# Optimization experiments

Hardware: AMD Instinct MI355X
Metric: run time of the kernel (lower is better)

## Reference

```python
import jax, jax.numpy as jnp
import numpy as np

N_NODES = 10000
N_EDGES = 320000
F_IN = 128


def _mlp2(h, W1, b1, W2, b2):
    h = jax.nn.relu(h @ W1 + b1)
    return jax.nn.relu(h @ W2 + b2)


def edge_conv(x, src, dst, W1, b1, W2, b2, num_nodes):
    # DGCNN-style EdgeConv: per-edge message MLP(concat(x_i, x_j - x_i)), max-agg per node i
    xi = x[dst]                      # [E, F] center node features
    xj = x[src]                      # [E, F] neighbor features
    m = jnp.concatenate([xi, xj - xi], axis=-1)  # [E, 2F]
    h = _mlp2(m, W1, b1, W2, b2)     # [E, F_out]
    agg = jax.ops.segment_max(h, dst, num_segments=num_nodes)  # [N, F_out]
    # nodes with no incoming edges get -inf from segment_max; zero them
    return jnp.where(jnp.isfinite(agg), agg, 0.0)


def setup_inputs() -> dict:
    key = jax.random.key(0)
    ks = jax.random.split(key, 16)
    s = 0.05
    x = jax.random.normal(ks[0], (N_NODES, F_IN), dtype=jnp.float32)
    edge_index = jax.random.randint(ks[1], (2, N_EDGES), 0, N_NODES)
    # EdgeConvE 1: MLP(512, 256), input 2*128=256
    W1a = jax.random.normal(ks[2], (2 * F_IN, 512), dtype=jnp.float32) * s
    b1a = jnp.zeros((512,), dtype=jnp.float32)
    W2a = jax.random.normal(ks[3], (512, 256), dtype=jnp.float32) * s
    b2a = jnp.zeros((256,), dtype=jnp.float32)
    # EdgeConvE 2: MLP(256, 128), input 2*256=512
    W1b = jax.random.normal(ks[4], (512, 256), dtype=jnp.float32) * s
    b1b = jnp.zeros((256,), dtype=jnp.float32)
    W2b = jax.random.normal(ks[5], (256, 128), dtype=jnp.float32) * s
    b2b = jnp.zeros((128,), dtype=jnp.float32)
    # Dense head
    W3 = jax.random.normal(ks[6], (128, 64), dtype=jnp.float32) * s
    b3 = jnp.zeros((64,), dtype=jnp.float32)
    W4 = jax.random.normal(ks[7], (64, 1), dtype=jnp.float32) * s
    b4 = jnp.zeros((1,), dtype=jnp.float32)
    return {"x": x, "edge_index": edge_index,
            "W1a": W1a, "b1a": b1a, "W2a": W2a, "b2a": b2a,
            "W1b": W1b, "b1b": b1b, "W2b": W2b, "b2b": b2b,
            "W3": W3, "b3": b3, "W4": W4, "b4": b4}


def reference(x, edge_index, W1a, b1a, W2a, b2a, W1b, b1b, W2b, b2b, W3, b3, W4, b4):
    src, dst = edge_index[0], edge_index[1]
    h = edge_conv(x, src, dst, W1a, b1a, W2a, b2a, N_NODES)   # [N, 256]
    h = edge_conv(h, src, dst, W1b, b1b, W2b, b2b, N_NODES)   # [N, 128]
    h = jax.nn.relu(h @ W3 + b3)                               # [N, 64]
    return jax.nn.sigmoid(h @ W4 + b4)                         # [N, 1]
```

## Files before the change

kernel.cpp:

```cpp
#include <hip/hip_runtime.h>
#include <math.h>

#define NN 10000
#define NE 320000

typedef __attribute__((ext_vector_type(8))) short s8v;
typedef __attribute__((ext_vector_type(8))) _Float16 h8v;
typedef __attribute__((ext_vector_type(4))) float f4v;

__device__ __forceinline__ short f2h(float f) {
  _Float16 h = (_Float16)f;
  short s; __builtin_memcpy(&s, &h, 2); return s;
}
__device__ __forceinline__ uint4 cvt8(uint4 ua, uint4 ub) {
  h8v a, b;
  __builtin_memcpy(&a, &ua, 16);
  __builtin_memcpy(&b, &ub, 16);
  h8v r = a + b;
  r = __builtin_elementwise_max(r, (h8v)(_Float16)0.0f);
  uint4 o; __builtin_memcpy(&o, &r, 16);
  return o;
}

__global__ void hist_kernel(const int* __restrict__ ei, int* __restrict__ cnt) {
  int e = blockIdx.x * 256 + threadIdx.x;
  if (e < NE) atomicAdd(&cnt[ei[NE + e]], 1);
}

__global__ void __launch_bounds__(1024)
scan_kernel(const int* __restrict__ cnt, int* __restrict__ cur) {
  __shared__ int part[1024];
  const int t = threadIdx.x;
  const int base = t * 10;
  int local[10];
  int s = 0;
#pragma unroll
  for (int u = 0; u < 10; ++u) {
    int c = (base + u < NN) ? cnt[base + u] : 0;
    local[u] = s; s += c;
  }
  part[t] = s;
  __syncthreads();
  for (int off = 1; off < 1024; off <<= 1) {
    int v = part[t];
    int w = (t >= off) ? part[t - off] : 0;
    __syncthreads();
    part[t] = v + w;
    __syncthreads();
  }
  int excl = (t == 0) ? 0 : part[t - 1];
#pragma unroll
  for (int u = 0; u < 10; ++u)
    if (base + u < NN) cur[base + u] = excl + local[u];
}

__global__ void scatter_kernel(const int* __restrict__ ei, int* __restrict__ cur,
                               int* __restrict__ sSrc, int* __restrict__ sDst) {
  int e = blockIdx.x * 256 + threadIdx.x;
  if (e < NE) {
    int d = ei[NE + e];
    int p = atomicAdd(&cur[d], 1);
    sSrc[p] = ei[e];
    sDst[p] = d;
  }
}

__global__ void prep_weights(const float* __restrict__ W1a, const float* __restrict__ W1b,
                             const float* __restrict__ W2a, const float* __restrict__ W2b,
                             short* __restrict__ Wp1T, short* __restrict__ Wp2T,
                             short* __restrict__ BTf1, short* __restrict__ BTf2) {
  int i = blockIdx.x * 256 + threadIdx.x;
  if (i < 131072) {
    int j = i >> 7, k = i & 127;
    float v;
    if (j < 512) v = W1a[k * 512 + j] - W1a[(k + 128) * 512 + j];
    else         v = W1a[(k + 128) * 512 + (j - 512)];
    Wp1T[i] = f2h(v);
  } else if (i < 262144) {
    int t = i - 131072;
    int j = t >> 8, k = t & 255;
    float v;
    if (j < 256) v = W1b[k * 256 + j] - W1b[(k + 256) * 256 + j];
    else         v = W1b[(k + 256) * 256 + (j - 256)];
    Wp2T[t] = f2h(v);
  } else if (i < 393216) {
    int t = i - 262144;
    int n = t >> 9, k = t & 511;
    BTf1[(k >> 5) * 8192 + n * 32 + (k & 31)] = f2h(W2a[k * 256 + n]);
  } else if (i < 425984) {
    int t = i - 393216;
    int n = t >> 8, k = t & 255;
    BTf2[(k >> 5) * 4096 + n * 32 + (k & 31)] = f2h(W2b[k * 128 + n]);
  }
}

template<int K>
__global__ void __launch_bounds__(256)
node_gemm(const float* __restrict__ A, const short* __restrict__ BT,
          const float* __restrict__ bias, int biasLen,
          short* __restrict__ C, int Ntot) {
  const int rowBase = blockIdx.x * 64;
  const int wave = threadIdx.x >> 6, lane = threadIdx.x & 63;
  const int colBase = blockIdx.y * 256 + wave * 64;
  const int lm = lane & 15, q = lane >> 4;
  f4v acc[4][4] = {};
  int arow[4];
#pragma unroll
  for (int mt = 0; mt < 4; ++mt) {
    int r = rowBase + mt * 16 + lm;
    arow[mt] = r < NN ? r : NN - 1;
  }
  for (int kk = 0; kk < K; kk += 32) {
    const int k = kk + q * 8;
    h8v aF[4], bF[4];
#pragma unroll
    for (int mt = 0; mt < 4; ++mt) {
      const float4* ap = (const float4*)(A + (size_t)arow[mt] * K + k);
      float4 x0 = ap[0], x1 = ap[1];
      h8v t;
      t[0] = (_Float16)x0.x; t[1] = (_Float16)x0.y; t[2] = (_Float16)x0.z; t[3] = (_Float16)x0.w;
      t[4] = (_Float16)x1.x; t[5] = (_Float16)x1.y; t[6] = (_Float16)x1.z; t[7] = (_Float16)x1.w;
      aF[mt] = t;
    }
#pragma unroll
    for (int nt = 0; nt < 4; ++nt)
      bF[nt] = *(const h8v*)(BT + (size_t)(colBase + nt * 16 + lm) * K + k);
#pragma unroll
    for (int mt = 0; mt < 4; ++mt)
#pragma unroll
      for (int nt = 0; nt < 4; ++nt)
        acc[mt][nt] = __builtin_amdgcn_mfma_f32_16x16x32_f16(aF[mt], bF[nt], acc[mt][nt], 0, 0, 0);
  }
#pragma unroll
  for (int nt = 0; nt < 4; ++nt) {
    int col = colBase + nt * 16 + lm;
    float bv = (col < biasLen) ? bias[col] : 0.0f;
#pragma unroll
    for (int mt = 0; mt < 4; ++mt) {
#pragma unroll
      for (int i = 0; i < 4; ++i) {
        int row = rowBase + mt * 16 + q * 4 + i;
        if (row < NN) C[(size_t)row * Ntot + col] = f2h(acc[mt][nt][i] + bv);
      }
    }
  }
}

template<int K, int NT>
__global__ void __launch_bounds__(512, 4)
edge_gemm_pf(const short* __restrict__ AB, const short* __restrict__ BTf,
             const float* __restrict__ bias,
             const int* __restrict__ sSrc, const int* __restrict__ sDst,
             int* __restrict__ y) {
  constexpr int ROWS = 128;
  constexpr int KT = 64;
  constexpr int KTP = 72;
  constexpr int TILES = K / KT;
  constexpr int WCOLS = NT / 4;
  constexpr int NTL = WCOLS / 16;
  __shared__ __align__(16) short hA[2][ROWS * KTP];
  __shared__ int srcS[ROWS], dstS[ROWS];
  __shared__ int segDst[2][64];
  __shared__ int segAtm[2][64];
  __shared__ __align__(4) unsigned char rowSidC[ROWS];
  __shared__ int segD[2];

  const int tid = threadIdx.x;
  const int eBase = blockIdx.x * ROWS;
  const int wave = tid >> 6, lane = tid & 63, lm = lane & 15, q = lane >> 4;
  const int cg = wave & 3, rg = wave >> 2;
  const int cBase = cg * WCOLS;
  const int rg64 = rg * 64;

  if (tid < ROWS) { srcS[tid] = sSrc[eBase + tid]; dstS[tid] = sDst[eBase + tid]; }
  __syncthreads();

  const int r0 = tid >> 3, kc0 = (tid & 7) * 8;
  const int r1 = r0 + 64;
  const size_t dO0 = (size_t)dstS[r0] * (2 * K) + kc0;
  const size_t sO0 = (size_t)srcS[r0] * (2 * K) + K + kc0;
  const size_t dO1 = (size_t)dstS[r1] * (2 * K) + kc0;
  const size_t sO1 = (size_t)srcS[r1] * (2 * K) + K + kc0;

  uint4 av0 = *(const uint4*)(AB + dO0);
  uint4 bv0 = *(const uint4*)(AB + sO0);
  uint4 av1 = *(const uint4*)(AB + dO1);
  uint4 bv1 = *(const uint4*)(AB + sO1);

  if (tid < 2 * 64) {
    const int w = tid >> 6;
    const int r = tid & 63;
    const int row = tid;
    int d = dstS[row];
    int prev = (r == 0) ? -1 : dstS[row - 1];
    bool flag = (r == 0) || (d != prev);
    unsigned long long mask = __ballot(flag);
    int Dtot = __popcll(mask);
    int sid = __popcll(mask & (0xFFFFFFFFFFFFFFFFull >> (63 - r))) - 1;
    rowSidC[row] = (unsigned char)sid;
    if (r == 0) segD[w] = Dtot;
    if (flag) {
      int prevOut = (w == 1) ? dstS[63]
                             : ((eBase > 0) ? sDst[eBase - 1] : -1);
      int nextOut = (w == 0) ? dstS[64]
                             : ((eBase + ROWS < NE) ? sDst[eBase + ROWS] : -1);
      bool atm = false;
      if (sid == 0 && prevOut == d) atm = true;
      if (sid == Dtot - 1 && nextOut == d) atm = true;
      segDst[w][sid] = d;
      segAtm[w][sid] = atm ? 1 : 0;
    }
  }

  f4v acc[4][NTL] = {};

  for (int t = 0; t < TILES; ++t) {
    h8v bF0[NTL];
#pragma unroll
    for (int nt = 0; nt < NTL; ++nt)
      bF0[nt] = *(const h8v*)(BTf + (size_t)(t * 2) * (NT * 32) +
                              (cBase + nt * 16 + lm) * 32 + q * 8);
    short* hbuf = hA[t & 1];
    {
      *(uint4*)(&hbuf[r0 * KTP + kc0]) = cvt8(av0, bv0);
      *(uint4*)(&hbuf[r1 * KTP + kc0]) = cvt8(av1, bv1);
    }
    if (t + 1 < TILES) {
      const int kn = (t + 1) * KT;
      av0 = *(const uint4*)(AB + dO0 + kn);
      bv0 = *(const uint4*)(AB + sO0 + kn);
      av1 = *(const uint4*)(AB + dO1 + kn);
      bv1 = *(const uint4*)(AB + sO1 + kn);
    }
    __syncthreads();
    {
      const int kl = q * 8;
      __builtin_amdgcn_s_setprio(1);
#pragma unroll
      for (int mt = 0; mt < 4; ++mt) {
        h8v aF = *(const h8v*)(&hbuf[(rg64 + mt * 16 + lm) * KTP + kl]);
#pragma unroll
        for (int nt = 0; nt < NTL; ++nt)
          acc[mt][nt] = __builtin_amdgcn_mfma_f32_16x16x32_f16(aF, bF0[nt], acc[mt][nt], 0, 0, 0);
      }
      __builtin_amdgcn_s_setprio(0);
    }
    {
      h8v bF1[NTL];
#pragma unroll
      for (int nt = 0; nt < NTL; ++nt)
        bF1[nt] = *(const h8v*)(BTf + (size_t)(t * 2 + 1) * (NT * 32) +
                                (cBase + nt * 16 + lm) * 32 + q * 8);
      const int kl = 32 + q * 8;
      __builtin_amdgcn_s_setprio(1);
#pragma unroll
      for (int mt = 0; mt < 4; ++mt) {
        h8v aF = *(const h8v*)(&hbuf[(rg64 + mt * 16 + lm) * KTP + kl]);
#pragma unroll
        for (int nt = 0; nt < NTL; ++nt)
          acc[mt][nt] = __builtin_amdgcn_mfma_f32_16x16x32_f16(aF, bF1[nt], acc[mt][nt], 0, 0, 0);
      }
      __builtin_amdgcn_s_setprio(0);
    }
  }

  const int D = segD[rg];
  int sid[4][4];
#pragma unroll
  for (int mt = 0; mt < 4; ++mt) {
    unsigned pk = *(const unsigned*)(&rowSidC[rg64 + mt * 16 + q * 4]);
#pragma unroll
    for (int i = 0; i < 4; ++i) sid[mt][i] = (int)((pk >> (8 * i)) & 255u);
  }
#pragma unroll
  for (int nt = 0; nt < NTL; ++nt) {
    const int col = cBase + nt * 16 + lm;
    const float bvv = bias[col];
    for (int s = 0; s < D; ++s) {
      float m = -1e30f;
#pragma unroll
      for (int mt = 0; mt < 4; ++mt)
#pragma unroll
        for (int i = 0; i < 4; ++i)
          m = fmaxf(m, sid[mt][i] == s ? acc[mt][nt][i] : -1e30f);
      m = fmaxf(m, __shfl_xor(m, 16));
      m = fmaxf(m, __shfl_xor(m, 32));
      if (q == 0) {
        float v = m + bvv;
        int* addr = &y[(size_t)segDst[rg][s] * NT + col];
        if (segAtm[rg][s]) {
          if (v > 0.f) atomicMax(addr, __float_as_int(v));
        } else {
          *addr = __float_as_int(fmaxf(v, 0.f));
        }
      }
    }
  }
}

__global__ void __launch_bounds__(64)
head_kernel(const float* __restrict__ y2, const float* __restrict__ W3,
            const float* __restrict__ b3, const float* __restrict__ W4,
            const float* __restrict__ b4, float* __restrict__ out) {
  const int n = blockIdx.x, j = threadIdx.x;
  const float* yr = y2 + (size_t)n * 128;
  float acc = 0.f;
#pragma unroll
  for (int k = 0; k < 128; ++k) acc += yr[k] * W3[k * 64 + j];
  acc += b3[j];
  float h = acc > 0.f ? acc : 0.f;
  float p = h * W4[j];
#pragma unroll
  for (int off = 32; off; off >>= 1) p += __shfl_down(p, off);
  if (j == 0) {
    float z = p + b4[0];
    out[n] = 1.f / (1.f + expf(-z));
  }
}

__global__ void diag_kernel(float* out, float v) { out[0] = v; }

extern "C" void kernel_launch(void* const* d_in, const int* in_sizes, int n_in,
                              void* d_out, int out_size, void* d_ws, size_t ws_size,
                              hipStream_t stream) {
  const float* x   = (const float*)d_in[0];
  const int*   ei  = (const int*)d_in[1];
  const float* W1a = (const float*)d_in[2];
  const float* b1a = (const float*)d_in[3];
  const float* W2a = (const float*)d_in[4];
  const float* b2a = (const float*)d_in[5];
  const float* W1b = (const float*)d_in[6];
  const float* b1b = (const float*)d_in[7];
  const float* W2b = (const float*)d_in[8];
  const float* b2b = (const float*)d_in[9];
  const float* W3  = (const float*)d_in[10];
  const float* b3  = (const float*)d_in[11];
  const float* W4  = (const float*)d_in[12];
  const float* b4  = (const float*)d_in[13];

  char* ws = (char*)d_ws;
  short* Wp1T = (short*)(ws + 0);
  short* Wp2T = (short*)(ws + 262144);
  short* BTf1 = (short*)(ws + 524288);
  short* BTf2 = (short*)(ws + 786432);
  short* A1B1 = (short*)(ws + 851968);
  short* A2B2 = (short*)(ws + 851968);
  int*   Y1   = (int*)(ws + 21331968);
  int*   Y2   = (int*)(ws + 21331968);
  int*   cnt  = (int*)(ws + 31571968);
  int*   cur  = (int*)(ws + 31611968);
  int*   sSrc = (int*)(ws + 31651968);
  int*   sDst = (int*)(ws + 32931968);

  if (ws_size < 34211968) {
    diag_kernel<<<1, 1, 0, stream>>>((float*)d_out, (float)ws_size);
    return;
  }

  hipMemsetAsync(cnt, 0, 40000, stream);
  hist_kernel<<<1250, 256, 0, stream>>>(ei, cnt);
  scan_kernel<<<1, 1024, 0, stream>>>(cnt, cur);
  scatter_kernel<<<1250, 256, 0, stream>>>(ei, cur, sSrc, sDst);

  prep_weights<<<1664, 256, 0, stream>>>(W1a, W1b, W2a, W2b, Wp1T, Wp2T, BTf1, BTf2);

  node_gemm<128><<<dim3(157, 4), 256, 0, stream>>>(x, Wp1T, b1a, 512, A1B1, 1024);
  hipMemsetAsync(Y1, 0, (size_t)NN * 256 * 4, stream);
  edge_gemm_pf<512, 256><<<2500, 512, 0, stream>>>(A1B1, BTf1, b2a, sSrc, sDst, Y1);

  node_gemm<256><<<dim3(157, 2), 256, 0, stream>>>((const float*)Y1, Wp2T, b1b, 256, A2B2, 512);
  hipMemsetAsync(Y2, 0, (size_t)NN * 128 * 4, stream);
  edge_gemm_pf<256, 128><<<2500, 512, 0, stream>>>(A2B2, BTf2, b2b, sSrc, sDst, Y2);

  head_kernel<<<NN, 64, 0, stream>>>((const float*)Y2, W3, b3, W4, b4, (float*)d_out);
}
```

Baseline: 404.0 us.

## Retile edge GEMM to 256-thread blocks and use LDS-only barrier waits

The edge GEMM kernel is parameterised by rows per block and now runs with 4 waves, each owning 64 output columns. Layer 1 uses 64-row blocks over 5000 blocks and layer 2 uses 128-row blocks. The per-tile __syncthreads is replaced by a barrier that waits only on LDS counters, so prefetch global loads can stay in flight across the barrier. This changes occupancy and per-wave register pressure, and a missing vmcnt wait before consuming prefetched registers relies on the compiler inserting one.

```diff
diff --git a/kernel.cpp b/kernel.cpp
--- a/kernel.cpp
+++ b/kernel.cpp
@@ -4,7 +4,6 @@
 #define NN 10000
 #define NE 320000
 
-typedef __attribute__((ext_vector_type(8))) short s8v;
 typedef __attribute__((ext_vector_type(8))) _Float16 h8v;
 typedef __attribute__((ext_vector_type(4))) float f4v;
 
@@ -20,6 +19,11 @@
   r = __builtin_elementwise_max(r, (h8v)(_Float16)0.0f);
   uint4 o; __builtin_memcpy(&o, &r, 16);
   return o;
+}
+
+__device__ __forceinline__ void barrier_lgkm_only() {
+  asm volatile("s_waitcnt lgkmcnt(0)" ::: "memory");
+  __builtin_amdgcn_s_barrier();
 }
 
 __global__ void hist_kernel(const int* __restrict__ ei, int* __restrict__ cnt) {
@@ -146,18 +150,20 @@
   }
 }
 
-template<int K, int NT>
-__global__ void __launch_bounds__(512, 4)
+template<int K, int NT, int ROWS>
+__global__ void __launch_bounds__(256, 3)
 edge_gemm_pf(const short* __restrict__ AB, const short* __restrict__ BTf,
              const float* __restrict__ bias,
              const int* __restrict__ sSrc, const int* __restrict__ sDst,
              int* __restrict__ y) {
-  constexpr int ROWS = 128;
   constexpr int KT = 64;
   constexpr int KTP = 72;
   constexpr int TILES = K / KT;
-  constexpr int WCOLS = NT / 4;
-  constexpr int NTL = WCOLS / 16;
+  constexpr int NCG = NT / 64;
+  constexpr int NRG = 4 / NCG;
+  constexpr int CH = ROWS / 32;
+  constexpr int NTL = 4;
+  static_assert(ROWS == 64 * NRG, "geometry");
   __shared__ __align__(16) short hA[2][ROWS * KTP];
   __shared__ int srcS[ROWS], dstS[ROWS];
   __shared__ int segDst[2][64];
@@ -168,26 +174,29 @@
   const int tid = threadIdx.x;
   const int eBase = blockIdx.x * ROWS;
   const int wave = tid >> 6, lane = tid & 63, lm = lane & 15, q = lane >> 4;
-  const int cg = wave & 3, rg = wave >> 2;
-  const int cBase = cg * WCOLS;
+  const int cg = wave % NCG, rg = wave / NCG;
+  const int cBase = cg * 64;
   const int rg64 = rg * 64;
 
   if (tid < ROWS) { srcS[tid] = sSrc[eBase + tid]; dstS[tid] = sDst[eBase + tid]; }
   __syncthreads();
 
   const int r0 = tid >> 3, kc0 = (tid & 7) * 8;
-  const int r1 = r0 + 64;
-  const size_t dO0 = (size_t)dstS[r0] * (2 * K) + kc0;
-  const size_t sO0 = (size_t)srcS[r0] * (2 * K) + K + kc0;
-  const size_t dO1 = (size_t)dstS[r1] * (2 * K) + kc0;
-  const size_t sO1 = (size_t)srcS[r1] * (2 * K) + K + kc0;
-
-  uint4 av0 = *(const uint4*)(AB + dO0);
-  uint4 bv0 = *(const uint4*)(AB + sO0);
-  uint4 av1 = *(const uint4*)(AB + dO1);
-  uint4 bv1 = *(const uint4*)(AB + sO1);
-
-  if (tid < 2 * 64) {
+  size_t dO[CH], sO[CH];
+#pragma unroll
+  for (int c = 0; c < CH; ++c) {
+    dO[c] = (size_t)dstS[r0 + 32 * c] * (2 * K) + kc0;
+    sO[c] = (size_t)srcS[r0 + 32 * c] * (2 * K) + K + kc0;
+  }
+
+  uint4 av[CH], bv[CH];
+#pragma unroll
+  for (int c = 0; c < CH; ++c) {
+    av[c] = *(const uint4*)(AB + dO[c]);
+    bv[c] = *(const uint4*)(AB + sO[c]);
+  }
+
+  if (tid < NRG * 64) {
     const int w = tid >> 6;
     const int r = tid & 63;
     const int row = tid;
@@ -200,10 +209,10 @@
     rowSidC[row] = (unsigned char)sid;
     if (r == 0) segD[w] = Dtot;
     if (flag) {
-      int prevOut = (w == 1) ? dstS[63]
-                             : ((eBase > 0) ? sDst[eBase - 1] : -1);
-      int nextOut = (w == 0) ? dstS[64]
-                             : ((eBase + ROWS < NE) ? sDst[eBase + ROWS] : -1);
+      int prevOut = (w > 0) ? dstS[w * 64 - 1]
+                            : ((eBase > 0) ? sDst[eBase - 1] : -1);
+      int nextOut = (w < NRG - 1) ? dstS[(w + 1) * 64]
+                                  : ((eBase + ROWS < NE) ? sDst[eBase + ROWS] : -1);
       bool atm = false;
       if (sid == 0 && prevOut == d) atm = true;
       if (sid == Dtot - 1 && nextOut == d) atm = true;
@@ -221,18 +230,18 @@
       bF0[nt] = *(const h8v*)(BTf + (size_t)(t * 2) * (NT * 32) +
                               (cBase + nt * 16 + lm) * 32 + q * 8);
     short* hbuf = hA[t & 1];
-    {
-      *(uint4*)(&hbuf[r0 * KTP + kc0]) = cvt8(av0, bv0);
-      *(uint4*)(&hbuf[r1 * KTP + kc0]) = cvt8(av1, bv1);
-    }
+#pragma unroll
+    for (int c = 0; c < CH; ++c)
+      *(uint4*)(&hbuf[(r0 + 32 * c) * KTP + kc0]) = cvt8(av[c], bv[c]);
     if (t + 1 < TILES) {
       const int kn = (t + 1) * KT;
-      av0 = *(const uint4*)(AB + dO0 + kn);
-      bv0 = *(const uint4*)(AB + sO0 + kn);
-      av1 = *(const uint4*)(AB + dO1 + kn);
-      bv1 = *(const uint4*)(AB + sO1 + kn);
-    }
-    __syncthreads();
+#pragma unroll
+      for (int c = 0; c < CH; ++c) {
+        av[c] = *(const uint4*)(AB + dO[c] + kn);
+        bv[c] = *(const uint4*)(AB + sO[c] + kn);
+      }
+    }
+    barrier_lgkm_only();
     {
       const int kl = q * 8;
       __builtin_amdgcn_s_setprio(1);
@@ -366,11 +375,11 @@
 
   node_gemm<128><<<dim3(157, 4), 256, 0, stream>>>(x, Wp1T, b1a, 512, A1B1, 1024);
   hipMemsetAsync(Y1, 0, (size_t)NN * 256 * 4, stream);
-  edge_gemm_pf<512, 256><<<2500, 512, 0, stream>>>(A1B1, BTf1, b2a, sSrc, sDst, Y1);
+  edge_gemm_pf<512, 256, 64><<<5000, 256, 0, stream>>>(A1B1, BTf1, b2a, sSrc, sDst, Y1);
 
   node_gemm<256><<<dim3(157, 2), 256, 0, stream>>>((const float*)Y1, Wp2T, b1b, 256, A2B2, 512);
   hipMemsetAsync(Y2, 0, (size_t)NN * 128 * 4, stream);
-  edge_gemm_pf<256, 128><<<2500, 512, 0, stream>>>(A2B2, BTf2, b2b, sSrc, sDst, Y2);
+  edge_gemm_pf<256, 128, 128><<<2500, 256, 0, stream>>>(A2B2, BTf2, b2b, sSrc, sDst, Y2);
 
   head_kernel<<<NN, 64, 0, stream>>>((const float*)Y2, W3, b3, W4, b4, (float*)d_out);
 }
```

Result: faster. 374.2 us (-7.4%).
